# Kernel tuning notes

Hardware: AMD Instinct MI355X
Metric: run time of the kernel (lower is better)

## Reference

```python
import jax, jax.numpy as jnp
import numpy as np

B, C, L, NLAB, EMB, NFREQ, D = 256, 64, 512, 10, 256, 9, 8
FIN, FH, FOUT = 4 * C, C, C
P_TOTAL = FIN * FH + FH + FH * FOUT + FOUT + FIN * FOUT + FOUT


def _leaky(x):
    return jax.nn.leaky_relu(x, 0.2)


def _conv1d(x, w, b=None, pad=0):
    y = jax.lax.conv_general_dilated(x, w, (1,), [(pad, pad)], dimension_numbers=('NCH', 'OIH', 'NCH'))
    return y if b is None else y + b[None, :, None]


def _res1d(x, w0, b0, w1, b1, ws=None, pad=1):
    # GAN-stability style residual block: out = shortcut(x) + 0.1 * conv1(act(conv0(act(x))))
    xs = _conv1d(x, ws) if ws is not None else x
    dx = _conv1d(_leaky(x), w0, b0, pad)
    dx = _conv1d(_leaky(dx), w1, b1, pad)
    return xs + 0.1 * dx


def _pos_enc():
    # sinusoidal positional encoding, 2*NFREQ channels over L positions
    p = np.arange(L, dtype=np.float32)
    f = (np.pi / 2.0 ** np.arange(NFREQ, dtype=np.float32))[:, None]
    pe = np.concatenate([np.sin(f * p), np.cos(f * p)], axis=0)  # [2*NFREQ, L]
    return jnp.asarray(pe)


def _sobel_kernels():
    s = np.array([1.0, 2.0, 1.0], np.float32)
    d = np.array([-1.0, 0.0, 1.0], np.float32)
    kx = np.einsum('i,j,k->ijk', d, s, s)
    ky = np.einsum('i,j,k->ijk', s, d, s)
    kz = np.einsum('i,j,k->ijk', s, s, d)
    return jnp.asarray(np.stack([kx, ky, kz]))  # [3, 3, 3, 3]


def _sin_sobel(x, k):
    # depthwise 3D sobel along each axis, sin of gradients, concat with input -> 4C channels
    outs = [x]
    for i in range(3):
        w = jnp.broadcast_to(k[i][None, None], (C, 1, 3, 3, 3))
        g = jax.lax.conv_general_dilated(x, w, (1, 1, 1), [(1, 1)] * 3,
                                         dimension_numbers=('NCDHW', 'OIDHW', 'NCDHW'),
                                         feature_group_count=C)
        outs.append(jnp.sin(g))
    return jnp.concatenate(outs, axis=1)


def _inst_norm(x):
    m = x.mean(axis=(2, 3, 4), keepdims=True)
    v = x.var(axis=(2, 3, 4), keepdims=True)
    return (x - m) * jax.lax.rsqrt(v + 1e-5)


def _dyna(x, p):
    # hypernet-generated per-sample 1x1x1 residual conv block
    b = x.shape[0]
    xf = x.reshape(b, FIN, D * D * D)
    o = FIN * FH
    wh = p[:, :o].reshape(b, FH, FIN)
    bh = p[:, o:o + FH]; o += FH
    wl = p[:, o:o + FH * FOUT].reshape(b, FOUT, FH); o += FH * FOUT
    bl = p[:, o:o + FOUT]; o += FOUT
    ws = p[:, o:o + FIN * FOUT].reshape(b, FOUT, FIN); o += FIN * FOUT
    bs = p[:, o:o + FOUT]
    xs = jnp.einsum('boi,bis->bos', ws, xf) + bs[:, :, None]
    dx = _leaky(jnp.einsum('bhi,bis->bhs', wh, xf) + bh[:, :, None])
    dx = jnp.einsum('boh,bhs->bos', wl, dx) + bl[:, :, None]
    return (xs + 0.1 * dx).reshape(b, FOUT, D, D, D)


def _forward(codes, y, fc_w, fc_b, in_w0, in_b0, in_w1, in_b1, in_ws, leak, hyper_w, hyper_b,
             out_w0, out_b0, out_w1, out_b1, l1_w0, l1_b0, l1_w1, l1_b1,
             l2_w0, l2_b0, l2_w1, l2_b1, l2_ws):
    b = codes.shape[0]
    yemb = jax.nn.one_hot(y, NLAB, dtype=codes.dtype) @ fc_w.T + fc_b
    yemb = yemb / jnp.maximum(jnp.linalg.norm(yemb, axis=1, keepdims=True), 1e-12)
    pe = jnp.broadcast_to(_pos_enc()[None], (b, 2 * NFREQ, L))
    x = jnp.concatenate([codes, pe], axis=1)  # [B, C+2*NFREQ, L]
    x = _res1d(x, in_w0, in_b0, in_w1, in_b1, ws=in_ws)
    x = x.reshape(b, C, D, D, D)
    leak_c = jnp.clip(leak, 0.001, 1000.0)
    p = yemb @ hyper_w.T + hyper_b  # per-sample dynamic conv params [B, P_TOTAL]
    k = _sobel_kernels()
    for _ in range(8):
        xn = _inst_norm(x)
        xn = _sin_sobel(xn, k)
        xn = _dyna(xn, p)
        x = x + leak_c * xn
    x = x.reshape(b, C, L)
    x = _res1d(x, out_w0, out_b0, out_w1, out_b1)
    code_idx = jnp.argmax(codes, axis=1).reshape(b * L)
    logits = x.transpose(0, 2, 1).reshape(b * L, C)
    logp = jax.nn.log_softmax(logits, axis=-1)
    loss_cent = -jnp.take_along_axis(logp, code_idx[:, None], axis=1).mean()
    lat = _res1d(x, l1_w0, l1_b0, l1_w1, l1_b1, pad=0)
    lat = _res1d(lat, l2_w0, l2_b0, l2_w1, l2_b1, ws=l2_ws, pad=0)
    return lat[:, 0, :], loss_cent


def setup_inputs() -> dict:
    key = jax.random.key(0)
    ks = jax.random.split(key, 16)
    w = lambda k, s: 0.02 * jax.random.normal(k, s, jnp.float32)
    z = lambda s: jnp.zeros(s, jnp.float32)
    CIN = C + 2 * NFREQ  # 82
    return {
        'codes': jax.random.normal(ks[0], (B, C, L), jnp.float32),
        'y': jax.random.randint(ks[1], (B,), 0, NLAB),
        'fc_w': w(ks[2], (EMB, NLAB)), 'fc_b': z((EMB,)),
        'in_w0': w(ks[3], (C, CIN, 3)), 'in_b0': z((C,)),
        'in_w1': w(ks[4], (C, C, 3)), 'in_b1': z((C,)),
        'in_ws': w(ks[5], (C, CIN, 1)),
        'leak': jnp.asarray(0.1, jnp.float32),
        'hyper_w': w(ks[6], (P_TOTAL, EMB)), 'hyper_b': z((P_TOTAL,)),
        'out_w0': w(ks[7], (C, C, 3)), 'out_b0': z((C,)),
        'out_w1': w(ks[8], (C, C, 3)), 'out_b1': z((C,)),
        'l1_w0': w(ks[9], (C, C, 1)), 'l1_b0': z((C,)),
        'l1_w1': w(ks[10], (C, C, 1)), 'l1_b1': z((C,)),
        'l2_w0': w(ks[11], (1, C, 1)), 'l2_b0': z((1,)),
        'l2_w1': w(ks[12], (1, 1, 1)), 'l2_b1': z((1,)),
        'l2_ws': w(ks[13], (1, C, 1)),
    }


def reference(codes, y, fc_w, fc_b, in_w0, in_b0, in_w1, in_b1, in_ws, leak, hyper_w, hyper_b,
              out_w0, out_b0, out_w1, out_b1, l1_w0, l1_b0, l1_w1, l1_b1,
              l2_w0, l2_b0, l2_w1, l2_b1, l2_ws):
    return _forward(codes, y, fc_w, fc_b, in_w0, in_b0, in_w1, in_b1, in_ws, leak, hyper_w, hyper_b,
                    out_w0, out_b0, out_w1, out_b1, l1_w0, l1_b0, l1_w1, l1_b1,
                    l2_w0, l2_b0, l2_w1, l2_b1, l2_ws)
```

## Files before the change

### kernel.cpp

```cpp
#include <hip/hip_runtime.h>

#define B_ 256
#define C_ 64
#define L_ 512
#define CIN_ 82
#define NFREQ_ 9
#define EMB_ 256
#define NLAB_ 10
#define PT_ 37056
#define OFF_BH 16384
#define OFF_WL 16448
#define OFF_BL 20544
#define OFF_WS 20608
#define OFF_BS 36992
#define PI_F 3.14159265358979323846f

typedef short bh8 __attribute__((ext_vector_type(8)));
typedef float f32x4 __attribute__((ext_vector_type(4)));

__device__ inline float lrelu(float v){ return v > 0.f ? v : 0.2f*v; }

__device__ inline unsigned short f2bf(float f){
  unsigned u = __float_as_uint(f);
  u += 0x7FFFu + ((u >> 16) & 1u);
  return (unsigned short)(u >> 16);
}
__device__ inline float bf2f(unsigned short u){
  return __uint_as_float((unsigned)u << 16);
}
__device__ inline unsigned pk2(float a, float b){
  return (unsigned)f2bf(a) | ((unsigned)f2bf(b) << 16);
}
__device__ inline bh8 cvt8(float4 a, float4 b){
  bh8 r;
  r[0]=(short)f2bf(a.x); r[1]=(short)f2bf(a.y); r[2]=(short)f2bf(a.z); r[3]=(short)f2bf(a.w);
  r[4]=(short)f2bf(b.x); r[5]=(short)f2bf(b.y); r[6]=(short)f2bf(b.z); r[7]=(short)f2bf(b.w);
  return r;
}
__device__ inline bh8 ld16_4(const unsigned short* p){
  union { unsigned u[4]; bh8 v; } t;
  t.u[0]=*(const unsigned*)p;     t.u[1]=*(const unsigned*)(p+2);
  t.u[2]=*(const unsigned*)(p+4); t.u[3]=*(const unsigned*)(p+6);
  return t.v;
}
__device__ inline bh8 ld8(const unsigned short* p){
  union { uint2 u[2]; bh8 v; } t;
  t.u[0] = *(const uint2*)p; t.u[1] = *(const uint2*)(p+4);
  return t.v;
}

__device__ inline int perm_j(int j){
  if (j < OFF_BH){ int m = j >> 8, i = j & 255; return (m << 8) + ((i & 63) << 2) + (i >> 6); }
  if (j >= OFF_WS && j < OFF_BS){
    int jj = j - OFF_WS; int m = jj >> 8, i = jj & 255;
    return OFF_WS + (m << 8) + ((i & 63) << 2) + (i >> 6);
  }
  return j;
}

__global__ __launch_bounds__(256) void k_yemb(const float* __restrict__ fc_w,
    const float* __restrict__ fc_b, const int* __restrict__ y,
    unsigned short* __restrict__ ybf, float* __restrict__ out){
  int b = blockIdx.x, e = threadIdx.x;
  int lab = y[b];
  float v = fc_w[e*NLAB_ + lab] + fc_b[e];
  __shared__ float red[256];
  red[e] = v*v; __syncthreads();
  for (int s = 128; s; s >>= 1){ if (e < s) red[e] += red[e+s]; __syncthreads(); }
  float nrm = fmaxf(sqrtf(red[0]), 1e-12f);
  ybf[(size_t)b*EMB_ + e] = f2bf(v / nrm);
  if (b == 0 && e == 0) out[B_*L_] = 0.f;
}

__global__ __launch_bounds__(256) void k_hyper(const float* __restrict__ hw,
    const float* __restrict__ hb, const unsigned short* __restrict__ ybf,
    unsigned short* __restrict__ p_bf){
  int tid = threadIdx.x;
  int wid = tid >> 6, lane = tid & 63, col = lane & 15, quad = lane >> 4;
  int j = blockIdx.x*64 + wid*16 + col;
  f32x4 acc[16];
  f32x4 z4 = {0.f,0.f,0.f,0.f};
  #pragma unroll
  for (int i = 0; i < 16; i++) acc[i] = z4;
  for (int k0 = 0; k0 < 256; k0 += 32){
    const float* hp = hw + (size_t)j*EMB_ + k0 + quad*8;
    bh8 bf = cvt8(*(const float4*)hp, *(const float4*)(hp+4));
    #pragma unroll
    for (int mt = 0; mt < 16; mt++){
      bh8 af = *(const bh8*)&ybf[(size_t)(mt*16 + col)*EMB_ + k0 + quad*8];
      acc[mt] = __builtin_amdgcn_mfma_f32_16x16x32_bf16(af, bf, acc[mt], 0, 0, 0);
    }
  }
  float hbv = hb[j];
  int jd = perm_j(j);
  #pragma unroll
  for (int mt = 0; mt < 16; mt++){
    int b0 = mt*16 + quad*4;
    #pragma unroll
    for (int r = 0; r < 4; r++)
      p_bf[(size_t)(b0 + r)*PT_ + jd] = f2bf(acc[mt][r] + hbv);
  }
}

__device__ inline float pe_raw(int fi, int l){
  if (fi < NFREQ_) return __sinf(PI_F / (float)(1 << fi) * (float)l);
  return __cosf(PI_F / (float)(1 << (fi - NFREQ_)) * (float)l);
}

__global__ __launch_bounds__(256) void k_conv_in1(const float* __restrict__ codes,
    const float* __restrict__ w0, const float* __restrict__ b0,
    unsigned short* __restrict__ t1bf){
  int b = blockIdx.x, l0 = blockIdx.y*128, tid = threadIdx.x;
  int wid = tid>>6, lane = tid&63, col = lane&15, quad = lane>>4;
  __shared__ __attribute__((aligned(16))) unsigned short xT[136][104];
  __shared__ __attribute__((aligned(16))) unsigned short wA[3][64][104];
  for (int i = tid; i < 64*96; i += 256){
    int m = i / 96, cin = i % 96;
    if (cin < CIN_){
      const float* s = w0 + (size_t)m*(CIN_*3) + cin*3;
      wA[0][m][cin] = f2bf(s[0]); wA[1][m][cin] = f2bf(s[1]); wA[2][m][cin] = f2bf(s[2]);
    } else { wA[0][m][cin] = 0; wA[1][m][cin] = 0; wA[2][m][cin] = 0; }
  }
  const float* cb = codes + (size_t)b*C_*L_;
  for (int i = tid; i < 96*34; i += 256){
    int c = i / 34, g = i % 34;
    int lg = l0 - 4 + 4*g;
    #pragma unroll
    for (int r2 = 0; r2 < 4; r2++){
      int l = lg + r2;
      float xv = 0.f;
      if (l >= 0 && l < L_){
        if (c < C_) xv = cb[(size_t)c*L_ + l];
        else if (c < CIN_) xv = pe_raw(c - C_, l);
      }
      xT[4*g + r2][c] = f2bf(lrelu(xv));
    }
  }
  __syncthreads();
  f32x4 z4 = {0.f,0.f,0.f,0.f};
  f32x4 acc[8];
  #pragma unroll
  for (int i = 0; i < 8; i++) acc[i] = z4;
  #pragma unroll
  for (int t = 0; t < 3; t++){
    #pragma unroll
    for (int k0 = 0; k0 < 96; k0 += 32){
      bh8 bfr[2];
      #pragma unroll
      for (int nt = 0; nt < 2; nt++)
        bfr[nt] = *(const bh8*)&xT[wid*32 + nt*16 + col + t + 3][k0 + quad*8];
      #pragma unroll
      for (int mt = 0; mt < 4; mt++){
        bh8 af = *(const bh8*)&wA[t][mt*16 + col][k0 + quad*8];
        #pragma unroll
        for (int nt = 0; nt < 2; nt++)
          acc[mt*2+nt] = __builtin_amdgcn_mfma_f32_16x16x32_bf16(af, bfr[nt], acc[mt*2+nt], 0,0,0);
      }
    }
  }
  #pragma unroll
  for (int mt = 0; mt < 4; mt++){
    int f0 = mt*16 + quad*4;
    float q0 = b0[f0], q1 = b0[f0+1], q2 = b0[f0+2], q3 = b0[f0+3];
    #pragma unroll
    for (int nt = 0; nt < 2; nt++){
      int l = l0 + wid*32 + nt*16 + col;
      f32x4 a = acc[mt*2+nt];
      uint2 o = { pk2(lrelu(a[0]+q0), lrelu(a[1]+q1)),
                  pk2(lrelu(a[2]+q2), lrelu(a[3]+q3)) };
      *(uint2*)&t1bf[((size_t)b*L_ + l)*64 + f0] = o;
    }
  }
}

__global__ __launch_bounds__(256) void k_conv_in2(const float* __restrict__ codes,
    const float* __restrict__ wsp, const float* __restrict__ w1, const float* __restrict__ b1,
    const unsigned short* __restrict__ t1bf, float* __restrict__ x){
  int b = blockIdx.x, l0 = blockIdx.y*128, tid = threadIdx.x;
  int wid = tid>>6, lane = tid&63, col = lane&15, quad = lane>>4;
  __shared__ __attribute__((aligned(16))) unsigned short xT[128][104];
  __shared__ __attribute__((aligned(16))) unsigned short wsA[64][104];
  __shared__ __attribute__((aligned(16))) unsigned short w1A[3][64][72];
  for (int i = tid; i < 64*96; i += 256){
    int m = i / 96, cin = i % 96;
    wsA[m][cin] = (cin < CIN_) ? f2bf(wsp[(size_t)m*CIN_ + cin]) : (unsigned short)0;
  }
  for (int i = tid; i < 64*64; i += 256){
    int m = i >> 6, cin = i & 63;
    const float* s = w1 + (size_t)m*192 + cin*3;
    w1A[0][m][cin] = f2bf(s[0]); w1A[1][m][cin] = f2bf(s[1]); w1A[2][m][cin] = f2bf(s[2]);
  }
  const float* cb = codes + (size_t)b*C_*L_;
  for (int i = tid; i < 96*32; i += 256){
    int c = i / 32, g = i % 32;
    int lg = l0 + 4*g;
    #pragma unroll
    for (int r2 = 0; r2 < 4; r2++){
      int l = lg + r2;
      float xv;
      if (c < C_) xv = cb[(size_t)c*L_ + l];
      else if (c < CIN_) xv = pe_raw(c - C_, l);
      else xv = 0.f;
      xT[4*g + r2][c] = f2bf(xv);
    }
  }
  __syncthreads();
  f32x4 z4 = {0.f,0.f,0.f,0.f};
  f32x4 accS[8], accD[8];
  #pragma unroll
  for (int i = 0; i < 8; i++){ accS[i] = z4; accD[i] = z4; }
  #pragma unroll
  for (int k0 = 0; k0 < 96; k0 += 32){
    bh8 bfr[2];
    #pragma unroll
    for (int nt = 0; nt < 2; nt++)
      bfr[nt] = *(const bh8*)&xT[wid*32 + nt*16 + col][k0 + quad*8];
    #pragma unroll
    for (int mt = 0; mt < 4; mt++){
      bh8 af = *(const bh8*)&wsA[mt*16 + col][k0 + quad*8];
      #pragma unroll
      for (int nt = 0; nt < 2; nt++)
        accS[mt*2+nt] = __builtin_amdgcn_mfma_f32_16x16x32_bf16(af, bfr[nt], accS[mt*2+nt], 0,0,0);
    }
  }
  bh8 zz8 = {0,0,0,0,0,0,0,0};
  #pragma unroll
  for (int t = 0; t < 3; t++){
    #pragma unroll
    for (int k0 = 0; k0 < 64; k0 += 32){
      bh8 bfr[2];
      #pragma unroll
      for (int nt = 0; nt < 2; nt++){
        int l = l0 + wid*32 + nt*16 + col + t - 1;
        bfr[nt] = (l >= 0 && l < L_)
          ? *(const bh8*)&t1bf[((size_t)b*L_ + l)*64 + k0 + quad*8] : zz8;
      }
      #pragma unroll
      for (int mt = 0; mt < 4; mt++){
        bh8 af = *(const bh8*)&w1A[t][mt*16 + col][k0 + quad*8];
        #pragma unroll
        for (int nt = 0; nt < 2; nt++)
          accD[mt*2+nt] = __builtin_amdgcn_mfma_f32_16x16x32_bf16(af, bfr[nt], accD[mt*2+nt], 0,0,0);
      }
    }
  }
  #pragma unroll
  for (int mt = 0; mt < 4; mt++){
    int f0 = mt*16 + quad*4;
    float q0 = b1[f0], q1 = b1[f0+1], q2 = b1[f0+2], q3 = b1[f0+3];
    #pragma unroll
    for (int nt = 0; nt < 2; nt++){
      int l = l0 + wid*32 + nt*16 + col;
      f32x4 s = accS[mt*2+nt], d = accD[mt*2+nt];
      size_t base = ((size_t)b*C_ + f0)*L_ + l;
      x[base]        = s[0] + 0.1f*(d[0] + q0);
      x[base + L_]   = s[1] + 0.1f*(d[1] + q1);
      x[base + 2*L_] = s[2] + 0.1f*(d[2] + q2);
      x[base + 3*L_] = s[3] + 0.1f*(d[3] + q3);
    }
  }
}

__global__ __launch_bounds__(512, 2) void k_iter(float* __restrict__ x,
    const unsigned short* __restrict__ p_bf, const float* __restrict__ leak){
  int b = blockIdx.x, tid = threadIdx.x;
  int wid = tid >> 6, lane = tid & 63, col = lane & 15, quad = lane >> 4;
  const unsigned short* pb = p_bf + (size_t)b*PT_;
  float* xb = x + (size_t)b*C_*L_;

  __shared__ __attribute__((aligned(16))) unsigned short h_t[512][68];
  unsigned short (*fch)[42] = (unsigned short (*)[42])&h_t[0][0];
  __shared__ float sm[64], sr[64];

  #pragma unroll
  for (int t = 0; t < 8; t++){
    int c = t*8 + wid;
    const float* xr = xb + (size_t)c*L_ + lane*8;
    float4 v0 = *(const float4*)xr, v1 = *(const float4*)(xr+4);
    float s1 = v0.x+v0.y+v0.z+v0.w + v1.x+v1.y+v1.z+v1.w;
    float s2 = v0.x*v0.x+v0.y*v0.y+v0.z*v0.z+v0.w*v0.w
             + v1.x*v1.x+v1.y*v1.y+v1.z*v1.z+v1.w*v1.w;
    #pragma unroll
    for (int m = 32; m; m >>= 1){ s1 += __shfl_xor(s1, m); s2 += __shfl_xor(s2, m); }
    if (lane == 0){
      float mean = s1 * (1.f/512.f);
      sm[c] = mean;
      sr[c] = rsqrtf(s2*(1.f/512.f) - mean*mean + 1e-5f);
    }
  }
  __syncthreads();

  f32x4 zz4 = {0.f,0.f,0.f,0.f};
  f32x4 acc_h[16], acc_s[16];
  #pragma unroll
  for (int i = 0; i < 16; i++){ acc_h[i] = zz4; acc_s[i] = zz4; }

  int yy = lane & 7;
  float wm = (yy > 0) ? 1.f : 0.f, wp = (yy < 7) ? 1.f : 0.f;
  float qm = (lane >= 8) ? 1.f : 0.f, qp = (lane < 56) ? 1.f : 0.f;

  for (int ch = 0; ch < 8; ch++){
    int c = ch*8 + wid;
    {
      const float* xr = xb + (size_t)c*L_ + lane*8;
      float4 v0 = *(const float4*)xr, v1 = *(const float4*)(xr+4);
      float r8[8] = { v0.x, v0.y, v0.z, v0.w, v1.x, v1.y, v1.z, v1.w };
      float mean = sm[c], rstd = sr[c];
      float xn[8];
      #pragma unroll
      for (int i = 0; i < 8; i++) xn[i] = (r8[i] - mean) * rstd;
      float A[8], Bv[8];
      A[0] = 2.f*xn[0] + xn[1];  Bv[0] = xn[1];
      #pragma unroll
      for (int i = 1; i < 7; i++){ A[i] = xn[i-1] + 2.f*xn[i] + xn[i+1]; Bv[i] = xn[i+1] - xn[i-1]; }
      A[7] = xn[6] + 2.f*xn[7];  Bv[7] = -xn[6];
      float Cv[8], Dv[8], Ev[8];
      #pragma unroll
      for (int i = 0; i < 8; i++){
        float am = __shfl_up(A[i], 1)*wm,  ap = __shfl_down(A[i], 1)*wp;
        float bm = __shfl_up(Bv[i], 1)*wm, bp = __shfl_down(Bv[i], 1)*wp;
        Cv[i] = am + 2.f*A[i] + ap;
        Dv[i] = ap - am;
        Ev[i] = bm + 2.f*Bv[i] + bp;
      }
      uint2 val[8];
      #pragma unroll
      for (int i = 0; i < 8; i++){
        float cm = __shfl_up(Cv[i], 8)*qm, cp = __shfl_down(Cv[i], 8)*qp;
        float dm = __shfl_up(Dv[i], 8)*qm, dp = __shfl_down(Dv[i], 8)*qp;
        float em = __shfl_up(Ev[i], 8)*qm, ep = __shfl_down(Ev[i], 8)*qp;
        float G0 = cp - cm;
        float G1 = dm + 2.f*Dv[i] + dp;
        float G2 = em + 2.f*Ev[i] + ep;
        val[i].x = pk2(xn[i], __sinf(G0));
        val[i].y = pk2(__sinf(G1), __sinf(G2));
      }
      int lrow = lane*8;
      #pragma unroll
      for (int j = 0; j < 8; j++){
        int i = (j + yy) & 7;
        unsigned short* dst = &fch[lrow + i][wid*4];
        *(unsigned*)dst       = val[i].x;
        *(unsigned*)(dst + 2) = val[i].y;
      }
    }
    __syncthreads();
    bh8 bfr[4];
    #pragma unroll
    for (int nt = 0; nt < 4; nt++)
      bfr[nt] = ld16_4(&fch[wid*64 + nt*16 + col][quad*8]);
    #pragma unroll
    for (int mt = 0; mt < 4; mt++){
      int m = mt*16 + col;
      bh8 ah = *(const bh8*)&pb[(size_t)m*256 + ch*32 + quad*8];
      bh8 aw = *(const bh8*)&pb[OFF_WS + (size_t)m*256 + ch*32 + quad*8];
      #pragma unroll
      for (int nt = 0; nt < 4; nt++){
        acc_h[mt*4+nt] = __builtin_amdgcn_mfma_f32_16x16x32_bf16(ah, bfr[nt], acc_h[mt*4+nt], 0, 0, 0);
        acc_s[mt*4+nt] = __builtin_amdgcn_mfma_f32_16x16x32_bf16(aw, bfr[nt], acc_s[mt*4+nt], 0, 0, 0);
      }
    }
    __syncthreads();
  }

  #pragma unroll
  for (int mt = 0; mt < 4; mt++){
    int f0 = mt*16 + quad*4;
    float bh0 = bf2f(pb[OFF_BH+f0]), bh1 = bf2f(pb[OFF_BH+f0+1]);
    float bh2 = bf2f(pb[OFF_BH+f0+2]), bh3 = bf2f(pb[OFF_BH+f0+3]);
    #pragma unroll
    for (int nt = 0; nt < 4; nt++){
      int n = wid*64 + nt*16 + col;
      f32x4 a = acc_h[mt*4+nt];
      uint2 o = { pk2(lrelu(a[0]+bh0), lrelu(a[1]+bh1)),
                  pk2(lrelu(a[2]+bh2), lrelu(a[3]+bh3)) };
      *(uint2*)&h_t[n][f0] = o;
    }
  }
  __syncthreads();
  f32x4 acc2[16];
  #pragma unroll
  for (int i = 0; i < 16; i++) acc2[i] = zz4;
  #pragma unroll
  for (int k0 = 0; k0 < 64; k0 += 32){
    bh8 hb[4];
    #pragma unroll
    for (int nt = 0; nt < 4; nt++)
      hb[nt] = ld8(&h_t[wid*64 + nt*16 + col][k0 + quad*8]);
    #pragma unroll
    for (int mt = 0; mt < 4; mt++){
      bh8 al = *(const bh8*)&pb[OFF_WL + (size_t)(mt*16 + col)*64 + k0 + quad*8];
      #pragma unroll
      for (int nt = 0; nt < 4; nt++)
        acc2[mt*4+nt] = __builtin_amdgcn_mfma_f32_16x16x32_bf16(al, hb[nt], acc2[mt*4+nt], 0, 0, 0);
    }
  }
  float lk = fminf(fmaxf(leak[0], 0.001f), 1000.f);
  int ncol = wid*64;
  #pragma unroll
  for (int mt = 0; mt < 4; mt++){
    int f0 = mt*16 + quad*4;
    float bs0 = bf2f(pb[OFF_BS+f0]), bs1 = bf2f(pb[OFF_BS+f0+1]);
    float bs2 = bf2f(pb[OFF_BS+f0+2]), bs3 = bf2f(pb[OFF_BS+f0+3]);
    float bl0 = bf2f(pb[OFF_BL+f0]), bl1 = bf2f(pb[OFF_BL+f0+1]);
    float bl2 = bf2f(pb[OFF_BL+f0+2]), bl3 = bf2f(pb[OFF_BL+f0+3]);
    #pragma unroll
    for (int nt = 0; nt < 4; nt++){
      int s = ncol + nt*16 + col;
      f32x4 xs = acc_s[mt*4+nt], dx = acc2[mt*4+nt];
      float ov0 = xs[0] + bs0 + 0.1f*(dx[0] + bl0);
      float ov1 = xs[1] + bs1 + 0.1f*(dx[1] + bl1);
      float ov2 = xs[2] + bs2 + 0.1f*(dx[2] + bl2);
      float ov3 = xs[3] + bs3 + 0.1f*(dx[3] + bl3);
      size_t xi = ((size_t)b*C_ + f0)*L_ + s;
      x[xi]          += lk*ov0;
      x[xi + L_]     += lk*ov1;
      x[xi + 2*L_]   += lk*ov2;
      x[xi + 3*L_]   += lk*ov3;
    }
  }
}

__global__ __launch_bounds__(256) void k_conv_out1(const float* __restrict__ x,
    const float* __restrict__ w, const float* __restrict__ bias,
    unsigned short* __restrict__ t1bf){
  int b = blockIdx.x, l0 = blockIdx.y*128, tid = threadIdx.x;
  int wid = tid>>6, lane = tid&63, col = lane&15, quad = lane>>4;
  __shared__ __attribute__((aligned(16))) unsigned short xT[136][72];
  __shared__ __attribute__((aligned(16))) unsigned short wA[3][64][72];
  for (int i = tid; i < 64*64; i += 256){
    int m = i >> 6, cin = i & 63;
    const float* s = w + (size_t)m*192 + cin*3;
    wA[0][m][cin] = f2bf(s[0]); wA[1][m][cin] = f2bf(s[1]); wA[2][m][cin] = f2bf(s[2]);
  }
  const float* xb = x + (size_t)b*C_*L_;
  for (int i = tid; i < 64*34; i += 256){
    int c = i / 34, g = i % 34;
    int lg = l0 - 4 + 4*g;
    if (lg >= 0 && lg + 3 < L_){
      float4 f = *(const float4*)&xb[(size_t)c*L_ + lg];
      xT[4*g  ][c] = f2bf(lrelu(f.x));
      xT[4*g+1][c] = f2bf(lrelu(f.y));
      xT[4*g+2][c] = f2bf(lrelu(f.z));
      xT[4*g+3][c] = f2bf(lrelu(f.w));
    } else {
      #pragma unroll
      for (int r2 = 0; r2 < 4; r2++){
        int l = lg + r2;
        float v = (l >= 0 && l < L_) ? xb[(size_t)c*L_ + l] : 0.f;
        xT[4*g + r2][c] = f2bf(lrelu(v));
      }
    }
  }
  __syncthreads();
  f32x4 z4 = {0.f,0.f,0.f,0.f};
  f32x4 acc[8];
  #pragma unroll
  for (int i = 0; i < 8; i++) acc[i] = z4;
  #pragma unroll
  for (int t = 0; t < 3; t++){
    #pragma unroll
    for (int k0 = 0; k0 < 64; k0 += 32){
      bh8 bfr[2];
      #pragma unroll
      for (int nt = 0; nt < 2; nt++)
        bfr[nt] = *(const bh8*)&xT[wid*32 + nt*16 + col + t + 3][k0 + quad*8];
      #pragma unroll
      for (int mt = 0; mt < 4; mt++){
        bh8 af = *(const bh8*)&wA[t][mt*16 + col][k0 + quad*8];
        #pragma unroll
        for (int nt = 0; nt < 2; nt++)
          acc[mt*2+nt] = __builtin_amdgcn_mfma_f32_16x16x32_bf16(af, bfr[nt], acc[mt*2+nt], 0,0,0);
      }
    }
  }
  #pragma unroll
  for (int mt = 0; mt < 4; mt++){
    int f0 = mt*16 + quad*4;
    float q0 = bias[f0], q1 = bias[f0+1], q2 = bias[f0+2], q3 = bias[f0+3];
    #pragma unroll
    for (int nt = 0; nt < 2; nt++){
      int l = l0 + wid*32 + nt*16 + col;
      f32x4 a = acc[mt*2+nt];
      uint2 o = { pk2(lrelu(a[0]+q0), lrelu(a[1]+q1)),
                  pk2(lrelu(a[2]+q2), lrelu(a[3]+q3)) };
      *(uint2*)&t1bf[((size_t)b*L_ + l)*64 + f0] = o;
    }
  }
}

__global__ __launch_bounds__(256) void k_conv_out2(float* __restrict__ x,
    const unsigned short* __restrict__ t1bf, const float* __restrict__ w,
    const float* __restrict__ bias){
  int b = blockIdx.x, l0 = blockIdx.y*256, tid = threadIdx.x;
  int wid = tid>>6, lane = tid&63, col = lane&15, quad = lane>>4;
  __shared__ __attribute__((aligned(16))) unsigned short wA[3][64][72];
  for (int i = tid; i < 64*64; i += 256){
    int m = i >> 6, cin = i & 63;
    const float* s = w + (size_t)m*192 + cin*3;
    wA[0][m][cin] = f2bf(s[0]); wA[1][m][cin] = f2bf(s[1]); wA[2][m][cin] = f2bf(s[2]);
  }
  __syncthreads();
  f32x4 z4 = {0.f,0.f,0.f,0.f};
  f32x4 acc[16];
  #pragma unroll
  for (int i = 0; i < 16; i++) acc[i] = z4;
  bh8 zz8 = {0,0,0,0,0,0,0,0};
  #pragma unroll
  for (int t = 0; t < 3; t++){
    #pragma unroll
    for (int k0 = 0; k0 < 64; k0 += 32){
      bh8 bfr[4];
      #pragma unroll
      for (int nt = 0; nt < 4; nt++){
        int l = l0 + wid*64 + nt*16 + col + t - 1;
        bfr[nt] = (l >= 0 && l < L_)
          ? *(const bh8*)&t1bf[((size_t)b*L_ + l)*64 + k0 + quad*8] : zz8;
      }
      #pragma unroll
      for (int mt = 0; mt < 4; mt++){
        bh8 af = *(const bh8*)&wA[t][mt*16 + col][k0 + quad*8];
        #pragma unroll
        for (int nt = 0; nt < 4; nt++)
          acc[mt*4+nt] = __builtin_amdgcn_mfma_f32_16x16x32_bf16(af, bfr[nt], acc[mt*4+nt], 0,0,0);
      }
    }
  }
  #pragma unroll
  for (int mt = 0; mt < 4; mt++){
    int f0 = mt*16 + quad*4;
    float q0 = bias[f0], q1 = bias[f0+1], q2 = bias[f0+2], q3 = bias[f0+3];
    #pragma unroll
    for (int nt = 0; nt < 4; nt++){
      int l = l0 + wid*64 + nt*16 + col;
      f32x4 a = acc[mt*4+nt];
      size_t base = ((size_t)b*C_ + f0)*L_ + l;
      x[base]        += 0.1f*(a[0] + q0);
      x[base + L_]   += 0.1f*(a[1] + q1);
      x[base + 2*L_] += 0.1f*(a[2] + q2);
      x[base + 3*L_] += 0.1f*(a[3] + q3);
    }
  }
}

__global__ __launch_bounds__(256) void k_loss(const float* __restrict__ x,
    const float* __restrict__ codes, float* __restrict__ out){
  int b = blockIdx.x;
  int l = blockIdx.y*256 + threadIdx.x;
  const float* xb = x + (size_t)b*C_*L_ + l;
  const float* cb = codes + (size_t)b*C_*L_ + l;
  float m = -1e30f, cm = -1e30f;
  int ci = 0;
  for (int c = 0; c < C_; c++){
    float xv = xb[(size_t)c*L_];
    m = fmaxf(m, xv);
    float cv = cb[(size_t)c*L_];
    if (cv > cm){ cm = cv; ci = c; }
  }
  float s = 0.f, vi = 0.f;
  for (int c = 0; c < C_; c++){
    float xv = xb[(size_t)c*L_];
    s += expf(xv - m);
    if (c == ci) vi = xv;
  }
  float lp = vi - m - logf(s);
  __shared__ float red[256];
  red[threadIdx.x] = -lp; __syncthreads();
  for (int sft = 128; sft; sft >>= 1){
    if (threadIdx.x < sft) red[threadIdx.x] += red[threadIdx.x + sft];
    __syncthreads();
  }
  if (threadIdx.x == 0) atomicAdd(out + B_*L_, red[0] * (1.0f/131072.0f));
}

__global__ __launch_bounds__(256) void k_lat(const float* __restrict__ x,
    const float* __restrict__ w10, const float* __restrict__ b10,
    const float* __restrict__ w11, const float* __restrict__ b11,
    const float* __restrict__ w20, const float* __restrict__ b20,
    const float* __restrict__ w21, const float* __restrict__ b21,
    const float* __restrict__ ws2, float* __restrict__ out){
  int b = blockIdx.x, l0 = blockIdx.y*256;
  int tid = threadIdx.x;
  int wid = tid >> 6, lane = tid & 63, col = lane & 15, quad = lane >> 4;
  __shared__ __attribute__((aligned(16))) unsigned short wA[2][64][72];
  __shared__ __attribute__((aligned(16))) unsigned short Bt[256][72];

  for (int i = tid; i < 1024; i += 256){
    int arr = i >> 9, rem = i & 511, row = rem >> 3, seg = rem & 7;
    const float* src = (arr ? w11 : w10) + (size_t)row*C_ + seg*8;
    *(bh8*)&wA[arr][row][seg*8] = cvt8(*(const float4*)src, *(const float4*)(src+4));
  }
  for (int i = tid; i < 4096; i += 256){
    int c = i >> 6, seg = i & 63;
    float4 v = *(const float4*)&x[((size_t)b*C_ + c)*L_ + l0 + seg*4];
    Bt[seg*4+0][c] = f2bf(lrelu(v.x));
    Bt[seg*4+1][c] = f2bf(lrelu(v.y));
    Bt[seg*4+2][c] = f2bf(lrelu(v.z));
    Bt[seg*4+3][c] = f2bf(lrelu(v.w));
  }
  __syncthreads();
  f32x4 z4 = {0.f,0.f,0.f,0.f};
  f32x4 acc1[16];
  #pragma unroll
  for (int i = 0; i < 16; i++) acc1[i] = z4;
  #pragma unroll
  for (int k0 = 0; k0 < 64; k0 += 32){
    bh8 bfr[4];
    #pragma unroll
    for (int nt = 0; nt < 4; nt++)
      bfr[nt] = *(const bh8*)&Bt[wid*64 + nt*16 + col][k0 + quad*8];
    #pragma unroll
    for (int mt = 0; mt < 4; mt++){
      bh8 af = *(const bh8*)&wA[0][mt*16 + col][k0 + quad*8];
      #pragma unroll
      for (int nt = 0; nt < 4; nt++)
        acc1[mt*4+nt] = __builtin_amdgcn_mfma_f32_16x16x32_bf16(af, bfr[nt], acc1[mt*4+nt], 0, 0, 0);
    }
  }
  #pragma unroll
  for (int mt = 0; mt < 4; mt++){
    int f0 = mt*16 + quad*4;
    f32x4 bv = *(const f32x4*)&b10[f0];
    #pragma unroll
    for (int nt = 0; nt < 4; nt++){
      int n = wid*64 + nt*16 + col;
      f32x4 a = acc1[mt*4+nt];
      uint2 o = { pk2(lrelu(a[0]+bv[0]), lrelu(a[1]+bv[1])),
                  pk2(lrelu(a[2]+bv[2]), lrelu(a[3]+bv[3])) };
      *(uint2*)&Bt[n][f0] = o;
    }
  }
  f32x4 acc2[16];
  #pragma unroll
  for (int i = 0; i < 16; i++) acc2[i] = z4;
  #pragma unroll
  for (int k0 = 0; k0 < 64; k0 += 32){
    bh8 bfr[4];
    #pragma unroll
    for (int nt = 0; nt < 4; nt++)
      bfr[nt] = *(const bh8*)&Bt[wid*64 + nt*16 + col][k0 + quad*8];
    #pragma unroll
    for (int mt = 0; mt < 4; mt++){
      bh8 af = *(const bh8*)&wA[1][mt*16 + col][k0 + quad*8];
      #pragma unroll
      for (int nt = 0; nt < 4; nt++)
        acc2[mt*4+nt] = __builtin_amdgcn_mfma_f32_16x16x32_bf16(af, bfr[nt], acc2[mt*4+nt], 0, 0, 0);
    }
  }
  float psA[4] = {0.f,0.f,0.f,0.f}, psB[4] = {0.f,0.f,0.f,0.f};
  #pragma unroll
  for (int mt = 0; mt < 4; mt++){
    int f0 = mt*16 + quad*4;
    f32x4 b11v = *(const f32x4*)&b11[f0];
    f32x4 wsv  = *(const f32x4*)&ws2[f0];
    f32x4 w20v = *(const f32x4*)&w20[f0];
    #pragma unroll
    for (int nt = 0; nt < 4; nt++){
      int lg = l0 + wid*64 + nt*16 + col;
      size_t base = ((size_t)b*C_ + f0)*L_ + lg;
      f32x4 a = acc2[mt*4+nt];
      #pragma unroll
      for (int r = 0; r < 4; r++){
        float xv = x[base + (size_t)r*L_];
        float lat = xv + 0.1f*(a[r] + b11v[r]);
        psA[nt] += wsv[r]*lat;
        psB[nt] += w20v[r]*lrelu(lat);
      }
    }
  }
  #pragma unroll
  for (int nt = 0; nt < 4; nt++){
    psA[nt] += __shfl_xor(psA[nt], 16); psA[nt] += __shfl_xor(psA[nt], 32);
    psB[nt] += __shfl_xor(psB[nt], 16); psB[nt] += __shfl_xor(psB[nt], 32);
  }
  if (quad == 0){
    float b20s = b20[0], w21s = w21[0], b21s = b21[0];
    #pragma unroll
    for (int nt = 0; nt < 4; nt++){
      float dx2 = w21s*lrelu(psB[nt] + b20s) + b21s;
      out[(size_t)b*L_ + l0 + wid*64 + nt*16 + col] = psA[nt] + 0.1f*dx2;
    }
  }
}

extern "C" void kernel_launch(void* const* d_in, const int* in_sizes, int n_in,
                              void* d_out, int out_size, void* d_ws, size_t ws_size,
                              hipStream_t stream) {
  (void)in_sizes; (void)n_in; (void)out_size; (void)ws_size;
  const float* codes   = (const float*)d_in[0];
  const int*   y       = (const int*)  d_in[1];
  const float* fc_w    = (const float*)d_in[2];
  const float* fc_b    = (const float*)d_in[3];
  const float* in_w0   = (const float*)d_in[4];
  const float* in_b0   = (const float*)d_in[5];
  const float* in_w1   = (const float*)d_in[6];
  const float* in_b1   = (const float*)d_in[7];
  const float* in_wsp  = (const float*)d_in[8];
  const float* leak    = (const float*)d_in[9];
  const float* hyper_w = (const float*)d_in[10];
  const float* hyper_b = (const float*)d_in[11];
  const float* out_w0  = (const float*)d_in[12];
  const float* out_b0  = (const float*)d_in[13];
  const float* out_w1  = (const float*)d_in[14];
  const float* out_b1  = (const float*)d_in[15];
  const float* l1_w0   = (const float*)d_in[16];
  const float* l1_b0   = (const float*)d_in[17];
  const float* l1_w1   = (const float*)d_in[18];
  const float* l1_b1   = (const float*)d_in[19];
  const float* l2_w0   = (const float*)d_in[20];
  const float* l2_b0   = (const float*)d_in[21];
  const float* l2_w1   = (const float*)d_in[22];
  const float* l2_b1   = (const float*)d_in[23];
  const float* l2_ws   = (const float*)d_in[24];
  float* out = (float*)d_out;

  char* ws = (char*)d_ws;
  unsigned short* p_bf = (unsigned short*)(ws);
  unsigned short* ybf  = (unsigned short*)(ws + 18972672);
  float* x             = (float*)(ws + 19103744);
  unsigned short* t1bf = (unsigned short*)(ws + 52658176);

  k_yemb<<<B_, 256, 0, stream>>>(fc_w, fc_b, y, ybf, out);
  k_hyper<<<PT_/64, 256, 0, stream>>>(hyper_w, hyper_b, ybf, p_bf);
  k_conv_in1<<<dim3(B_, 4), 256, 0, stream>>>(codes, in_w0, in_b0, t1bf);
  k_conv_in2<<<dim3(B_, 4), 256, 0, stream>>>(codes, in_wsp, in_w1, in_b1, t1bf, x);
  for (int it = 0; it < 8; ++it){
    k_iter<<<B_, 512, 0, stream>>>(x, p_bf, leak);
  }
  k_conv_out1<<<dim3(B_, 4), 256, 0, stream>>>(x, out_w0, out_b0, t1bf);
  k_conv_out2<<<dim3(B_, 2), 256, 0, stream>>>(x, t1bf, out_w1, out_b1);
  k_loss<<<dim3(B_, 2), 256, 0, stream>>>(x, codes, out);
  k_lat<<<dim3(B_, 2), 256, 0, stream>>>(x, l1_w0, l1_b0, l1_w1, l1_b1,
                                         l2_w0, l2_b0, l2_w1, l2_b1, l2_ws, out);
}
```

Measured before the change: 926.4 us.

## Double k_iter block to 16 waves with 32-column tiles and fused Sobel shuffles

The per-sample iteration kernel now runs 1024 threads (16 waves) instead of 512. Each wave handles 32 spatial columns, and each channel chunk covers 16 channels with two K-steps of MFMA, which halves the per-thread accumulator count. The two Sobel shuffle loops are merged so the intermediate arrays are not kept live, and the staging buffer now uses the full 68-wide h_t row with 8-byte stores. The goal is more waves in flight to hide latency, at the cost of losing the explicit two-blocks-per-CU occupancy hint and paying barrier cost across more waves.

```diff
diff --git a/kernel.cpp b/kernel.cpp
--- a/kernel.cpp
+++ b/kernel.cpp
@@ -37,12 +37,6 @@
   r[4]=(short)f2bf(b.x); r[5]=(short)f2bf(b.y); r[6]=(short)f2bf(b.z); r[7]=(short)f2bf(b.w);
   return r;
 }
-__device__ inline bh8 ld16_4(const unsigned short* p){
-  union { unsigned u[4]; bh8 v; } t;
-  t.u[0]=*(const unsigned*)p;     t.u[1]=*(const unsigned*)(p+2);
-  t.u[2]=*(const unsigned*)(p+4); t.u[3]=*(const unsigned*)(p+6);
-  return t.v;
-}
 __device__ inline bh8 ld8(const unsigned short* p){
   union { uint2 u[2]; bh8 v; } t;
   t.u[0] = *(const uint2*)p; t.u[1] = *(const uint2*)(p+4);
@@ -261,7 +255,7 @@
   }
 }
 
-__global__ __launch_bounds__(512, 2) void k_iter(float* __restrict__ x,
+__global__ __launch_bounds__(1024) void k_iter(float* __restrict__ x,
     const unsigned short* __restrict__ p_bf, const float* __restrict__ leak){
   int b = blockIdx.x, tid = threadIdx.x;
   int wid = tid >> 6, lane = tid & 63, col = lane & 15, quad = lane >> 4;
@@ -269,12 +263,11 @@
   float* xb = x + (size_t)b*C_*L_;
 
   __shared__ __attribute__((aligned(16))) unsigned short h_t[512][68];
-  unsigned short (*fch)[42] = (unsigned short (*)[42])&h_t[0][0];
   __shared__ float sm[64], sr[64];
 
   #pragma unroll
-  for (int t = 0; t < 8; t++){
-    int c = t*8 + wid;
+  for (int t = 0; t < 4; t++){
+    int c = t*16 + wid;
     const float* xr = xb + (size_t)c*L_ + lane*8;
     float4 v0 = *(const float4*)xr, v1 = *(const float4*)(xr+4);
     float s1 = v0.x+v0.y+v0.z+v0.w + v1.x+v1.y+v1.z+v1.w;
@@ -291,16 +284,16 @@
   __syncthreads();
 
   f32x4 zz4 = {0.f,0.f,0.f,0.f};
-  f32x4 acc_h[16], acc_s[16];
-  #pragma unroll
-  for (int i = 0; i < 16; i++){ acc_h[i] = zz4; acc_s[i] = zz4; }
+  f32x4 acc_h[8], acc_s[8];
+  #pragma unroll
+  for (int i = 0; i < 8; i++){ acc_h[i] = zz4; acc_s[i] = zz4; }
 
   int yy = lane & 7;
   float wm = (yy > 0) ? 1.f : 0.f, wp = (yy < 7) ? 1.f : 0.f;
   float qm = (lane >= 8) ? 1.f : 0.f, qp = (lane < 56) ? 1.f : 0.f;
 
-  for (int ch = 0; ch < 8; ch++){
-    int c = ch*8 + wid;
+  for (int ch = 0; ch < 4; ch++){
+    int c = ch*16 + wid;
     {
       const float* xr = xb + (size_t)c*L_ + lane*8;
       float4 v0 = *(const float4*)xr, v1 = *(const float4*)(xr+4);
@@ -314,24 +307,20 @@
       #pragma unroll
       for (int i = 1; i < 7; i++){ A[i] = xn[i-1] + 2.f*xn[i] + xn[i+1]; Bv[i] = xn[i+1] - xn[i-1]; }
       A[7] = xn[6] + 2.f*xn[7];  Bv[7] = -xn[6];
-      float Cv[8], Dv[8], Ev[8];
+      uint2 val[8];
       #pragma unroll
       for (int i = 0; i < 8; i++){
         float am = __shfl_up(A[i], 1)*wm,  ap = __shfl_down(A[i], 1)*wp;
         float bm = __shfl_up(Bv[i], 1)*wm, bp = __shfl_down(Bv[i], 1)*wp;
-        Cv[i] = am + 2.f*A[i] + ap;
-        Dv[i] = ap - am;
-        Ev[i] = bm + 2.f*Bv[i] + bp;
-      }
-      uint2 val[8];
-      #pragma unroll
-      for (int i = 0; i < 8; i++){
-        float cm = __shfl_up(Cv[i], 8)*qm, cp = __shfl_down(Cv[i], 8)*qp;
-        float dm = __shfl_up(Dv[i], 8)*qm, dp = __shfl_down(Dv[i], 8)*qp;
-        float em = __shfl_up(Ev[i], 8)*qm, ep = __shfl_down(Ev[i], 8)*qp;
+        float Cv = am + 2.f*A[i] + ap;
+        float Dv = ap - am;
+        float Ev = bm + 2.f*Bv[i] + bp;
+        float cm = __shfl_up(Cv, 8)*qm, cp = __shfl_down(Cv, 8)*qp;
+        float dm = __shfl_up(Dv, 8)*qm, dp = __shfl_down(Dv, 8)*qp;
+        float em = __shfl_up(Ev, 8)*qm, ep = __shfl_down(Ev, 8)*qp;
         float G0 = cp - cm;
-        float G1 = dm + 2.f*Dv[i] + dp;
-        float G2 = em + 2.f*Ev[i] + ep;
+        float G1 = dm + 2.f*Dv + dp;
+        float G2 = em + 2.f*Ev + ep;
         val[i].x = pk2(xn[i], __sinf(G0));
         val[i].y = pk2(__sinf(G1), __sinf(G2));
       }
@@ -339,25 +328,26 @@
       #pragma unroll
       for (int j = 0; j < 8; j++){
         int i = (j + yy) & 7;
-        unsigned short* dst = &fch[lrow + i][wid*4];
-        *(unsigned*)dst       = val[i].x;
-        *(unsigned*)(dst + 2) = val[i].y;
+        *(uint2*)&h_t[lrow + i][wid*4] = val[i];
       }
     }
     __syncthreads();
-    bh8 bfr[4];
-    #pragma unroll
-    for (int nt = 0; nt < 4; nt++)
-      bfr[nt] = ld16_4(&fch[wid*64 + nt*16 + col][quad*8]);
-    #pragma unroll
-    for (int mt = 0; mt < 4; mt++){
-      int m = mt*16 + col;
-      bh8 ah = *(const bh8*)&pb[(size_t)m*256 + ch*32 + quad*8];
-      bh8 aw = *(const bh8*)&pb[OFF_WS + (size_t)m*256 + ch*32 + quad*8];
-      #pragma unroll
-      for (int nt = 0; nt < 4; nt++){
-        acc_h[mt*4+nt] = __builtin_amdgcn_mfma_f32_16x16x32_bf16(ah, bfr[nt], acc_h[mt*4+nt], 0, 0, 0);
-        acc_s[mt*4+nt] = __builtin_amdgcn_mfma_f32_16x16x32_bf16(aw, bfr[nt], acc_s[mt*4+nt], 0, 0, 0);
+    #pragma unroll
+    for (int kk = 0; kk < 2; kk++){
+      bh8 bfr[2];
+      #pragma unroll
+      for (int nt = 0; nt < 2; nt++)
+        bfr[nt] = ld8(&h_t[wid*32 + nt*16 + col][kk*32 + quad*8]);
+      #pragma unroll
+      for (int mt = 0; mt < 4; mt++){
+        int m = mt*16 + col;
+        bh8 ah = *(const bh8*)&pb[(size_t)m*256 + ch*64 + kk*32 + quad*8];
+        bh8 aw = *(const bh8*)&pb[OFF_WS + (size_t)m*256 + ch*64 + kk*32 + quad*8];
+        #pragma unroll
+        for (int nt = 0; nt < 2; nt++){
+          acc_h[mt*2+nt] = __builtin_amdgcn_mfma_f32_16x16x32_bf16(ah, bfr[nt], acc_h[mt*2+nt], 0, 0, 0);
+          acc_s[mt*2+nt] = __builtin_amdgcn_mfma_f32_16x16x32_bf16(aw, bfr[nt], acc_s[mt*2+nt], 0, 0, 0);
+        }
       }
     }
     __syncthreads();
@@ -369,34 +359,34 @@
     float bh0 = bf2f(pb[OFF_BH+f0]), bh1 = bf2f(pb[OFF_BH+f0+1]);
     float bh2 = bf2f(pb[OFF_BH+f0+2]), bh3 = bf2f(pb[OFF_BH+f0+3]);
     #pragma unroll
-    for (int nt = 0; nt < 4; nt++){
-      int n = wid*64 + nt*16 + col;
-      f32x4 a = acc_h[mt*4+nt];
+    for (int nt = 0; nt < 2; nt++){
+      int n = wid*32 + nt*16 + col;
+      f32x4 a = acc_h[mt*2+nt];
       uint2 o = { pk2(lrelu(a[0]+bh0), lrelu(a[1]+bh1)),
                   pk2(lrelu(a[2]+bh2), lrelu(a[3]+bh3)) };
       *(uint2*)&h_t[n][f0] = o;
     }
   }
   __syncthreads();
-  f32x4 acc2[16];
-  #pragma unroll
-  for (int i = 0; i < 16; i++) acc2[i] = zz4;
+  f32x4 acc2[8];
+  #pragma unroll
+  for (int i = 0; i < 8; i++) acc2[i] = zz4;
   #pragma unroll
   for (int k0 = 0; k0 < 64; k0 += 32){
-    bh8 hb[4];
-    #pragma unroll
-    for (int nt = 0; nt < 4; nt++)
-      hb[nt] = ld8(&h_t[wid*64 + nt*16 + col][k0 + quad*8]);
+    bh8 hb[2];
+    #pragma unroll
+    for (int nt = 0; nt < 2; nt++)
+      hb[nt] = ld8(&h_t[wid*32 + nt*16 + col][k0 + quad*8]);
     #pragma unroll
     for (int mt = 0; mt < 4; mt++){
       bh8 al = *(const bh8*)&pb[OFF_WL + (size_t)(mt*16 + col)*64 + k0 + quad*8];
       #pragma unroll
-      for (int nt = 0; nt < 4; nt++)
-        acc2[mt*4+nt] = __builtin_amdgcn_mfma_f32_16x16x32_bf16(al, hb[nt], acc2[mt*4+nt], 0, 0, 0);
+      for (int nt = 0; nt < 2; nt++)
+        acc2[mt*2+nt] = __builtin_amdgcn_mfma_f32_16x16x32_bf16(al, hb[nt], acc2[mt*2+nt], 0, 0, 0);
     }
   }
   float lk = fminf(fmaxf(leak[0], 0.001f), 1000.f);
-  int ncol = wid*64;
+  int ncol = wid*32;
   #pragma unroll
   for (int mt = 0; mt < 4; mt++){
     int f0 = mt*16 + quad*4;
@@ -405,9 +395,9 @@
     float bl0 = bf2f(pb[OFF_BL+f0]), bl1 = bf2f(pb[OFF_BL+f0+1]);
     float bl2 = bf2f(pb[OFF_BL+f0+2]), bl3 = bf2f(pb[OFF_BL+f0+3]);
     #pragma unroll
-    for (int nt = 0; nt < 4; nt++){
+    for (int nt = 0; nt < 2; nt++){
       int s = ncol + nt*16 + col;
-      f32x4 xs = acc_s[mt*4+nt], dx = acc2[mt*4+nt];
+      f32x4 xs = acc_s[mt*2+nt], dx = acc2[mt*2+nt];
       float ov0 = xs[0] + bs0 + 0.1f*(dx[0] + bl0);
       float ov1 = xs[1] + bs1 + 0.1f*(dx[1] + bl1);
       float ov2 = xs[2] + bs2 + 0.1f*(dx[2] + bl2);
@@ -725,7 +715,7 @@
   k_conv_in1<<<dim3(B_, 4), 256, 0, stream>>>(codes, in_w0, in_b0, t1bf);
   k_conv_in2<<<dim3(B_, 4), 256, 0, stream>>>(codes, in_wsp, in_w1, in_b1, t1bf, x);
   for (int it = 0; it < 8; ++it){
-    k_iter<<<B_, 512, 0, stream>>>(x, p_bf, leak);
+    k_iter<<<B_, 1024, 0, stream>>>(x, p_bf, leak);
   }
   k_conv_out1<<<dim3(B_, 4), 256, 0, stream>>>(x, out_w0, out_b0, t1bf);
   k_conv_out2<<<dim3(B_, 2), 256, 0, stream>>>(x, t1bf, out_w1, out_b1);
```

After: 1.021 ms. 10.2% more time.
